# Optimization experiments

Measured on AMD Instinct MI355X. Metric: run time of the kernel, lower is better.

Reference implementation:

```python
import jax, jax.numpy as jnp
import numpy as np

BATCH = 4096
DIM = 512
TEMP = 0.1

def setup_inputs() -> dict:
    key = jax.random.key(0)
    k1, k2 = jax.random.split(key)
    emb_i = jax.random.normal(k1, (BATCH, DIM), dtype=jnp.float32)
    emb_j = jax.random.normal(k2, (BATCH, DIM), dtype=jnp.float32)
    return {"emb_i": emb_i, "emb_j": emb_j}

def _l2_normalize(x, eps=1e-12):
    # matches torch F.normalize(dim=1): x / max(||x||, eps)
    norm = jnp.sqrt(jnp.sum(x * x, axis=1, keepdims=True))
    return x / jnp.maximum(norm, eps)

def reference(emb_i, emb_j):
    n = emb_i.shape[0]
    z_i = _l2_normalize(emb_i)
    z_j = _l2_normalize(emb_j)
    reps = jnp.concatenate([z_i, z_j], axis=0)  # [2N, D], rows unit-norm
    # cosine similarity of unit vectors == dot product -> GEMM instead of O(N^2 D) broadcast
    sim = reps @ reps.T  # [2N, 2N]
    # positives: diag offsets +N and -N
    pos_ij = jnp.sum(z_i * z_j, axis=1)  # diag(sim, +N)
    pos_ji = pos_ij                      # diag(sim, -N) is identical by symmetry
    positives = jnp.concatenate([pos_ij, pos_ji], axis=0)  # [2N]
    nominator = jnp.exp(positives / TEMP)
    neg_mask = 1.0 - jnp.eye(2 * n, dtype=sim.dtype)
    denominator = jnp.sum(neg_mask * jnp.exp(sim / TEMP), axis=1)  # [2N]
    loss_partial = -jnp.log(nominator / denominator)
    return jnp.sum(loss_partial) / (2 * n)
```

## Files before the change

kernel.cpp:

```cpp
#include <hip/hip_runtime.h>
#include <hip/hip_bf16.h>

#define N_ROWS 4096
#define DIM    512
#define M_ROWS 8192
#define BK     32
#define EXP_SCALE 14.4269504088896340736f

typedef unsigned short ushort_t;
typedef __attribute__((ext_vector_type(8))) short short8;
typedef __attribute__((ext_vector_type(4))) float f32x4;

__device__ __forceinline__ ushort_t f2bf(float x) {
  unsigned int bits = __float_as_uint(x);
  unsigned int lsb = (bits >> 16) & 1u;
  bits += 0x7fffu + lsb;
  return (ushort_t)(bits >> 16);
}

__device__ __forceinline__ void store4bf(ushort_t* p, float4 v, float s) {
  union { ushort_t u[4]; uint2 d; } pk;
  pk.u[0] = f2bf(v.x * s);
  pk.u[1] = f2bf(v.y * s);
  pk.u[2] = f2bf(v.z * s);
  pk.u[3] = f2bf(v.w * s);
  *(uint2*)p = pk.d;
}

__device__ __forceinline__ void async16(const ushort_t* g, ushort_t* l) {
  __builtin_amdgcn_global_load_lds(
      (const __attribute__((address_space(1))) void*)g,
      (__attribute__((address_space(3))) void*)l,
      16, 0, 0);
}

__global__ __launch_bounds__(64) void norm_kernel(
    const float* __restrict__ ei, const float* __restrict__ ej,
    ushort_t* __restrict__ reps, float* __restrict__ pos) {
  int b = blockIdx.x;
  int lane = threadIdx.x;
  const float4* pi = (const float4*)(ei + (size_t)b * DIM);
  const float4* pj = (const float4*)(ej + (size_t)b * DIM);
  float4 a0 = pi[lane];
  float4 a1 = pi[lane + 64];
  float4 b0 = pj[lane];
  float4 b1 = pj[lane + 64];

  float si = a0.x*a0.x + a0.y*a0.y + a0.z*a0.z + a0.w*a0.w
           + a1.x*a1.x + a1.y*a1.y + a1.z*a1.z + a1.w*a1.w;
  float sj = b0.x*b0.x + b0.y*b0.y + b0.z*b0.z + b0.w*b0.w
           + b1.x*b1.x + b1.y*b1.y + b1.z*b1.z + b1.w*b1.w;
  float dp = a0.x*b0.x + a0.y*b0.y + a0.z*b0.z + a0.w*b0.w
           + a1.x*b1.x + a1.y*b1.y + a1.z*b1.z + a1.w*b1.w;

#pragma unroll
  for (int m = 32; m >= 1; m >>= 1) {
    si += __shfl_xor(si, m, 64);
    sj += __shfl_xor(sj, m, 64);
    dp += __shfl_xor(dp, m, 64);
  }
  float ii = 1.0f / fmaxf(sqrtf(si), 1e-12f);
  float ij = 1.0f / fmaxf(sqrtf(sj), 1e-12f);
  if (lane == 0) pos[b] = dp * ii * ij;

  ushort_t* ri = reps + (size_t)b * DIM;
  ushort_t* rj = reps + (size_t)(b + N_ROWS) * DIM;
  store4bf(ri + lane * 4,       a0, ii);
  store4bf(ri + 256 + lane * 4, a1, ii);
  store4bf(rj + lane * 4,       b0, ij);
  store4bf(rj + 256 + lane * 4, b1, ij);
}

__global__ __launch_bounds__(256) void sim_kernel(
    const ushort_t* __restrict__ reps, float* __restrict__ denom) {
  int bj = blockIdx.x, bi = blockIdx.y;
  if (bi > bj) return;

  __shared__ ushort_t As[128 * BK];
  __shared__ ushort_t Bs[128 * BK];

  int tid  = threadIdx.x;
  int wave = tid >> 6, lane = tid & 63;
  int wr = wave >> 1, wc = wave & 1;
  int quad = lane >> 4, l15 = lane & 15;

  int c0 = wave * 2, c1 = c0 + 1;
  int srow  = lane >> 2;
  int selem = (lane & 3) * 8;
  const ushort_t* gA0 = reps + (size_t)(bi * 128 + c0 * 16 + srow) * DIM + selem;
  const ushort_t* gA1 = reps + (size_t)(bi * 128 + c1 * 16 + srow) * DIM + selem;
  const ushort_t* gB0 = reps + (size_t)(bj * 128 + c0 * 16 + srow) * DIM + selem;
  const ushort_t* gB1 = reps + (size_t)(bj * 128 + c1 * 16 + srow) * DIM + selem;
  ushort_t* lA0 = As + c0 * 512;
  ushort_t* lA1 = As + c1 * 512;
  ushort_t* lB0 = Bs + c0 * 512;
  ushort_t* lB1 = Bs + c1 * 512;

  f32x4 zero4 = {0.0f, 0.0f, 0.0f, 0.0f};
  f32x4 acc[4][4];
#pragma unroll
  for (int tr = 0; tr < 4; ++tr)
#pragma unroll
    for (int tc = 0; tc < 4; ++tc) acc[tr][tc] = zero4;

  for (int kk = 0; kk < DIM; kk += BK) {
    __syncthreads();
    async16(gA0 + kk, lA0);
    async16(gA1 + kk, lA1);
    async16(gB0 + kk, lB0);
    async16(gB1 + kk, lB1);
    __syncthreads();

    short8 aF[4], bF[4];
#pragma unroll
    for (int t = 0; t < 4; ++t) {
      aF[t] = *(const short8*)(As + (wr * 64 + t * 16 + l15) * BK + quad * 8);
      bF[t] = *(const short8*)(Bs + (wc * 64 + t * 16 + l15) * BK + quad * 8);
    }
#pragma unroll
    for (int tr = 0; tr < 4; ++tr)
#pragma unroll
      for (int tc = 0; tc < 4; ++tc)
        acc[tr][tc] = __builtin_amdgcn_mfma_f32_16x16x32_bf16(
            aF[tr], bF[tc], acc[tr][tc], 0, 0, 0);
  }

  int rowg_base = bi * 128 + wr * 64;
  int colg_base = bj * 128 + wc * 64;

  f32x4 rsum[4];
  float csum[4] = {0.0f, 0.0f, 0.0f, 0.0f};
#pragma unroll
  for (int tr = 0; tr < 4; ++tr) rsum[tr] = zero4;

#pragma unroll
  for (int tr = 0; tr < 4; ++tr) {
    int rowg0 = rowg_base + tr * 16 + quad * 4;
#pragma unroll
    for (int tc = 0; tc < 4; ++tc) {
      int colg = colg_base + tc * 16 + l15;
      f32x4 a = acc[tr][tc];
      f32x4 e;
#pragma unroll
      for (int r = 0; r < 4; ++r) {
        float v = exp2f(a[r] * EXP_SCALE);
        e[r] = ((rowg0 + r) == colg) ? 0.0f : v;
      }
      rsum[tr] += e;
      csum[tc] += e[0] + e[1] + e[2] + e[3];
    }
  }

#pragma unroll
  for (int m = 1; m <= 8; m <<= 1)
#pragma unroll
    for (int tr = 0; tr < 4; ++tr)
#pragma unroll
      for (int r = 0; r < 4; ++r)
        rsum[tr][r] += __shfl_xor(rsum[tr][r], m, 64);

  if (l15 == 0) {
#pragma unroll
    for (int tr = 0; tr < 4; ++tr)
#pragma unroll
      for (int r = 0; r < 4; ++r)
        atomicAdd(&denom[rowg_base + tr * 16 + quad * 4 + r], rsum[tr][r]);
  }

  if (bi != bj) {
#pragma unroll
    for (int m = 16; m <= 32; m <<= 1)
#pragma unroll
      for (int tc = 0; tc < 4; ++tc)
        csum[tc] += __shfl_xor(csum[tc], m, 64);
    if (quad == 0) {
#pragma unroll
      for (int tc = 0; tc < 4; ++tc)
        atomicAdd(&denom[colg_base + tc * 16 + l15], csum[tc]);
    }
  }
}

__global__ __launch_bounds__(256) void loss_kernel(
    const float* __restrict__ denom, const float* __restrict__ pos,
    float* __restrict__ out) {
  __shared__ float red[4];
  int tid = threadIdx.x;
  float p = 0.0f;
  for (int r = tid; r < M_ROWS; r += 256)
    p += logf(denom[r]) - pos[r & (N_ROWS - 1)] * 10.0f;
#pragma unroll
  for (int m = 32; m >= 1; m >>= 1) p += __shfl_xor(p, m, 64);
  if ((tid & 63) == 0) red[tid >> 6] = p;
  __syncthreads();
  if (tid == 0)
    out[0] = (red[0] + red[1] + red[2] + red[3]) * (1.0f / M_ROWS);
}

extern "C" void kernel_launch(void* const* d_in, const int* in_sizes, int n_in,
                              void* d_out, int out_size, void* d_ws, size_t ws_size,
                              hipStream_t stream) {
  const float* ei = (const float*)d_in[0];
  const float* ej = (const float*)d_in[1];
  float* out = (float*)d_out;

  char* ws = (char*)d_ws;
  ushort_t* reps = (ushort_t*)ws;
  float* denom = (float*)(ws + (size_t)M_ROWS * DIM * 2);
  float* pos = (float*)(ws + (size_t)M_ROWS * DIM * 2 + M_ROWS * 4);

  hipMemsetAsync(denom, 0, M_ROWS * sizeof(float), stream);
  norm_kernel<<<N_ROWS, 64, 0, stream>>>(ei, ej, reps, pos);
  sim_kernel<<<dim3(64, 64), 256, 0, stream>>>(reps, denom);
  loss_kernel<<<1, 256, 0, stream>>>(denom, pos, out);
}
```

Before: 156.6 us.

## Fuse memset and loss into kernels, drop LDS staging, compact triangular grid

Removes the hipMemsetAsync and the separate loss kernel. The denominator zeroing and counter reset move into the normalization kernel, which now processes 4 rows per 256-thread block. The last sim block, detected with an atomic counter, computes the final loss. The sim kernel launches only the 2080 upper-triangular tiles through index decoding instead of early-exiting half of a 64x64 grid. It also loads MFMA fragments straight from global memory into registers with double buffering, replacing LDS staging and syncthreads. The risk is that direct global loads are uncoalesced and lose the tile sharing that LDS gave across waves, which could raise memory traffic.

```diff
diff --git a/kernel.cpp b/kernel.cpp
--- a/kernel.cpp
+++ b/kernel.cpp
@@ -4,7 +4,8 @@
 #define N_ROWS 4096
 #define DIM    512
 #define M_ROWS 8192
-#define BK     32
+#define NTILE  64
+#define NBLK   2080
 #define EXP_SCALE 14.4269504088896340736f
 
 typedef unsigned short ushort_t;
@@ -27,18 +28,16 @@
   *(uint2*)p = pk.d;
 }
 
-__device__ __forceinline__ void async16(const ushort_t* g, ushort_t* l) {
-  __builtin_amdgcn_global_load_lds(
-      (const __attribute__((address_space(1))) void*)g,
-      (__attribute__((address_space(3))) void*)l,
-      16, 0, 0);
-}
-
-__global__ __launch_bounds__(64) void norm_kernel(
+__global__ __launch_bounds__(256) void norm_kernel(
     const float* __restrict__ ei, const float* __restrict__ ej,
-    ushort_t* __restrict__ reps, float* __restrict__ pos) {
-  int b = blockIdx.x;
-  int lane = threadIdx.x;
+    ushort_t* __restrict__ reps, float* __restrict__ pos,
+    float* __restrict__ denom, int* __restrict__ counter) {
+  int tid = threadIdx.x;
+  if (blockIdx.x < 32) denom[blockIdx.x * 256 + tid] = 0.0f;
+  if (blockIdx.x == 32 && tid == 0) *counter = 0;
+
+  int b = blockIdx.x * 4 + (tid >> 6);
+  int lane = tid & 63;
   const float4* pi = (const float4*)(ei + (size_t)b * DIM);
   const float4* pj = (const float4*)(ej + (size_t)b * DIM);
   float4 a0 = pi[lane];
@@ -72,29 +71,22 @@
 }
 
 __global__ __launch_bounds__(256) void sim_kernel(
-    const ushort_t* __restrict__ reps, float* __restrict__ denom) {
-  int bj = blockIdx.x, bi = blockIdx.y;
-  if (bi > bj) return;
-
-  __shared__ ushort_t As[128 * BK];
-  __shared__ ushort_t Bs[128 * BK];
+    const ushort_t* __restrict__ reps, float* __restrict__ denom,
+    const float* __restrict__ pos, float* __restrict__ out,
+    int* __restrict__ counter) {
+  int t = blockIdx.x;
+  int bi = (int)((129.0f - sqrtf((float)(16641 - 8 * t))) * 0.5f);
+  while (bi * (129 - bi) / 2 > t) --bi;
+  while ((bi + 1) * (128 - bi) / 2 <= t) ++bi;
+  int bj = bi + (t - bi * (129 - bi) / 2);
 
   int tid  = threadIdx.x;
   int wave = tid >> 6, lane = tid & 63;
   int wr = wave >> 1, wc = wave & 1;
   int quad = lane >> 4, l15 = lane & 15;
 
-  int c0 = wave * 2, c1 = c0 + 1;
-  int srow  = lane >> 2;
-  int selem = (lane & 3) * 8;
-  const ushort_t* gA0 = reps + (size_t)(bi * 128 + c0 * 16 + srow) * DIM + selem;
-  const ushort_t* gA1 = reps + (size_t)(bi * 128 + c1 * 16 + srow) * DIM + selem;
-  const ushort_t* gB0 = reps + (size_t)(bj * 128 + c0 * 16 + srow) * DIM + selem;
-  const ushort_t* gB1 = reps + (size_t)(bj * 128 + c1 * 16 + srow) * DIM + selem;
-  ushort_t* lA0 = As + c0 * 512;
-  ushort_t* lA1 = As + c1 * 512;
-  ushort_t* lB0 = Bs + c0 * 512;
-  ushort_t* lB1 = Bs + c1 * 512;
+  const short8* gA = (const short8*)(reps + (size_t)(bi * 128 + wr * 64 + l15) * DIM) + quad;
+  const short8* gB = (const short8*)(reps + (size_t)(bj * 128 + wc * 64 + l15) * DIM) + quad;
 
   f32x4 zero4 = {0.0f, 0.0f, 0.0f, 0.0f};
   f32x4 acc[4][4];
@@ -103,26 +95,41 @@
 #pragma unroll
     for (int tc = 0; tc < 4; ++tc) acc[tr][tc] = zero4;
 
-  for (int kk = 0; kk < DIM; kk += BK) {
-    __syncthreads();
-    async16(gA0 + kk, lA0);
-    async16(gA1 + kk, lA1);
-    async16(gB0 + kk, lB0);
-    async16(gB1 + kk, lB1);
-    __syncthreads();
-
-    short8 aF[4], bF[4];
-#pragma unroll
-    for (int t = 0; t < 4; ++t) {
-      aF[t] = *(const short8*)(As + (wr * 64 + t * 16 + l15) * BK + quad * 8);
-      bF[t] = *(const short8*)(Bs + (wc * 64 + t * 16 + l15) * BK + quad * 8);
+  short8 aE[4], bE[4], aO[4], bO[4];
+#pragma unroll
+  for (int x = 0; x < 4; ++x) {
+    aE[x] = gA[x * 1024];
+    bE[x] = gB[x * 1024];
+  }
+
+#pragma unroll
+  for (int k = 0; k < 16; k += 2) {
+    if (k + 1 < 16) {
+#pragma unroll
+      for (int x = 0; x < 4; ++x) {
+        aO[x] = gA[x * 1024 + (k + 1) * 4];
+        bO[x] = gB[x * 1024 + (k + 1) * 4];
+      }
     }
 #pragma unroll
     for (int tr = 0; tr < 4; ++tr)
 #pragma unroll
       for (int tc = 0; tc < 4; ++tc)
         acc[tr][tc] = __builtin_amdgcn_mfma_f32_16x16x32_bf16(
-            aF[tr], bF[tc], acc[tr][tc], 0, 0, 0);
+            aE[tr], bE[tc], acc[tr][tc], 0, 0, 0);
+    if (k + 2 < 16) {
+#pragma unroll
+      for (int x = 0; x < 4; ++x) {
+        aE[x] = gA[x * 1024 + (k + 2) * 4];
+        bE[x] = gB[x * 1024 + (k + 2) * 4];
+      }
+    }
+#pragma unroll
+    for (int tr = 0; tr < 4; ++tr)
+#pragma unroll
+      for (int tc = 0; tc < 4; ++tc)
+        acc[tr][tc] = __builtin_amdgcn_mfma_f32_16x16x32_bf16(
+            aO[tr], bO[tc], acc[tr][tc], 0, 0, 0);
   }
 
   int rowg_base = bi * 128 + wr * 64;
@@ -179,22 +186,26 @@
         atomicAdd(&denom[colg_base + tc * 16 + l15], csum[tc]);
     }
   }
-}
-
-__global__ __launch_bounds__(256) void loss_kernel(
-    const float* __restrict__ denom, const float* __restrict__ pos,
-    float* __restrict__ out) {
+
+  __shared__ int islast;
   __shared__ float red[4];
-  int tid = threadIdx.x;
-  float p = 0.0f;
-  for (int r = tid; r < M_ROWS; r += 256)
-    p += logf(denom[r]) - pos[r & (N_ROWS - 1)] * 10.0f;
-#pragma unroll
-  for (int m = 32; m >= 1; m >>= 1) p += __shfl_xor(p, m, 64);
-  if ((tid & 63) == 0) red[tid >> 6] = p;
+  __threadfence();
   __syncthreads();
-  if (tid == 0)
-    out[0] = (red[0] + red[1] + red[2] + red[3]) * (1.0f / M_ROWS);
+  if (tid == 0) islast = (atomicAdd(counter, 1) == NBLK - 1);
+  __syncthreads();
+  if (islast) {
+    float p = 0.0f;
+    for (int r = tid; r < M_ROWS; r += 256) {
+      float v = atomicAdd(&denom[r], 0.0f);
+      p += logf(v) - pos[r & (N_ROWS - 1)] * 10.0f;
+    }
+#pragma unroll
+    for (int m = 32; m >= 1; m >>= 1) p += __shfl_xor(p, m, 64);
+    if ((tid & 63) == 0) red[tid >> 6] = p;
+    __syncthreads();
+    if (tid == 0)
+      out[0] = (red[0] + red[1] + red[2] + red[3]) * (1.0f / M_ROWS);
+  }
 }
 
 extern "C" void kernel_launch(void* const* d_in, const int* in_sizes, int n_in,
@@ -208,9 +219,8 @@
   ushort_t* reps = (ushort_t*)ws;
   float* denom = (float*)(ws + (size_t)M_ROWS * DIM * 2);
   float* pos = (float*)(ws + (size_t)M_ROWS * DIM * 2 + M_ROWS * 4);
-
-  hipMemsetAsync(denom, 0, M_ROWS * sizeof(float), stream);
-  norm_kernel<<<N_ROWS, 64, 0, stream>>>(ei, ej, reps, pos);
-  sim_kernel<<<dim3(64, 64), 256, 0, stream>>>(reps, denom);
-  loss_kernel<<<1, 256, 0, stream>>>(denom, pos, out);
-}
+  int* counter = (int*)(ws + (size_t)M_ROWS * DIM * 2 + M_ROWS * 4 + N_ROWS * 4);
+
+  norm_kernel<<<N_ROWS / 4, 256, 0, stream>>>(ei, ej, reps, pos, denom, counter);
+  sim_kernel<<<NBLK, 256, 0, stream>>>(reps, denom, pos, out, counter);
+}
```

Result: slower. 345.5 us (+120.6%).
